# Kernel optimization log

Measured on AMD Instinct MI355X. Metric: run time of the kernel, lower is better.

The kernel has to match this reference:

```python
import jax, jax.numpy as jnp
import numpy as np

B = 16          # graphs per batch
NN = 2000       # nodes per graph (num_nodes)
N = B * NN      # total nodes in the batched graph
F_IN = 128      # input node features
H, C = 4, 64    # heads, per-head out channels (both GAT layers)
HC = H * C
DEG = 12        # average degree per node
FC1, FC2, OUT = 512, 128, 1
FC_IN = 6 * NN  # len(which_layer) = 6


def setup_inputs() -> dict:
    key = jax.random.key(0)
    ks = jax.random.split(key, 32)

    def g(i, shape, s=0.05):
        return jax.random.normal(ks[i], shape, jnp.float32) * s

    # within-graph random edges, no self loops (GATConv removes then re-adds them)
    src_l = jax.random.randint(ks[0], (B, NN * DEG), 0, NN)
    off = jax.random.randint(ks[1], (B, NN * DEG), 1, NN)
    dst_l = (src_l + off) % NN
    goff = (jnp.arange(B) * NN)[:, None]
    edge_index = jnp.stack([(src_l + goff).reshape(-1),
                            (dst_l + goff).reshape(-1)]).astype(jnp.int32)

    return {
        "x": g(2, (N, F_IN), 1.0),
        "W1": g(3, (F_IN, HC)), "att_src1": g(4, (H, C)), "att_dst1": g(5, (H, C)),
        "b1": jnp.zeros((HC,), jnp.float32),
        "W2": g(6, (HC, HC)), "att_src2": g(7, (H, C)), "att_dst2": g(8, (H, C)),
        "b2": jnp.zeros((HC,), jnp.float32),
        "pw1": g(9, (HC, 1)), "pb1": jnp.zeros((1,), jnp.float32),
        "pw2": g(10, (HC, 1)), "pb2": jnp.zeros((1,), jnp.float32),
        "ln_w": jnp.ones((NN,), jnp.float32), "ln_b": jnp.zeros((NN,), jnp.float32),
        "sex_emb": g(11, (2, NN)), "mut_emb": g(12, (4, NN)),
        "age_w": g(13, (NN,)), "age_b": jnp.zeros((NN,), jnp.float32),
        "fw1": g(14, (FC_IN, FC1)), "fb1": jnp.zeros((FC1,), jnp.float32),
        "fw2": g(15, (FC1, FC2)), "fb2": jnp.zeros((FC2,), jnp.float32),
        "fw3": g(16, (FC2, OUT)), "fb3": jnp.zeros((OUT,), jnp.float32),
        "age": jax.random.uniform(ks[17], (B,), jnp.float32),
        "edge_index": edge_index,
        "sex": jax.random.randint(ks[18], (B,), 0, 2),
        "mutation": jax.random.randint(ks[19], (B,), 0, 4),
    }


def _layer_norm(x, w, b, eps=1e-5):
    mu = jnp.mean(x, -1, keepdims=True)
    var = jnp.mean((x - mu) ** 2, -1, keepdims=True)
    return (x - mu) / jnp.sqrt(var + eps) * w + b


def _gat_conv(x, W, att_src, att_dst, bias, src, dst):
    h = (x @ W).reshape(N, H, C)                         # [N,H,C]
    a_s = jnp.sum(h * att_src[None], -1)                 # [N,H]
    a_d = jnp.sum(h * att_dst[None], -1)                 # [N,H]
    alpha = jax.nn.leaky_relu(a_s[src] + a_d[dst], 0.2)  # [E,H]
    m = jax.ops.segment_max(alpha, dst, num_segments=N)  # segment softmax over dst
    e = jnp.exp(alpha - m[dst])
    denom = jax.ops.segment_sum(e, dst, num_segments=N)
    a = e / (denom[dst] + 1e-16)
    out = jax.ops.segment_sum(a[:, :, None] * h[src], dst, num_segments=N)
    return out.reshape(N, HC) + bias


def _forward(x, W1, att_src1, att_dst1, b1, W2, att_src2, att_dst2, b2,
             pw1, pb1, pw2, pb2, ln_w, ln_b, sex_emb, mut_emb, age_w, age_b,
             fw1, fb1, fw2, fb2, fw3, fb3, age, edge_index, sex, mutation):
    loop = jnp.arange(N, dtype=edge_index.dtype)         # self loops added by GATConv
    src = jnp.concatenate([edge_index[0], loop])
    dst = jnp.concatenate([edge_index[1], loop])

    x0 = jnp.mean(x, -1).reshape(B, NN)                  # to_dense_batch(mean(x,-1))

    h = jax.nn.relu(_gat_conv(x, W1, att_src1, att_dst1, b1, src, dst))
    x1 = (h @ pw1 + pb1).squeeze(-1).reshape(B, NN)
    h = jax.nn.relu(_gat_conv(h, W2, att_src2, att_dst2, b2, src, dst))
    x2 = (h @ pw2 + pb2).squeeze(-1).reshape(B, NN)

    x0 = _layer_norm(x0, ln_w, ln_b)
    x1 = _layer_norm(x1, ln_w, ln_b)
    x2 = _layer_norm(x2, ln_w, ln_b)
    ms = jnp.concatenate([x0, x1, x2], axis=1)           # [B, 3*NN]

    demo = jnp.concatenate([sex_emb[sex], mut_emb[mutation],
                            age[:, None] * age_w[None, :] + age_b], axis=1)
    t = jnp.concatenate([demo, ms], axis=1)              # [B, 6*NN]
    t = jax.nn.relu(t @ fw1 + fb1)
    t = jax.nn.relu(t @ fw2 + fb2)
    pred = t @ fw3 + fb3                                 # [B, 1]
    return pred, x0, x1, x2, ms


def reference(x, W1, att_src1, att_dst1, b1, W2, att_src2, att_dst2, b2,
              pw1, pb1, pw2, pb2, ln_w, ln_b, sex_emb, mut_emb, age_w, age_b,
              fw1, fb1, fw2, fb2, fw3, fb3, age, edge_index, sex, mutation):
    return _forward(x, W1, att_src1, att_dst1, b1, W2, att_src2, att_dst2, b2,
                    pw1, pb1, pw2, pb2, ln_w, ln_b, sex_emb, mut_emb, age_w, age_b,
                    fw1, fb1, fw2, fb2, fw3, fb3, age, edge_index, sex, mutation)
```

## Files before the change

kernel.cpp:

```cpp
#include <hip/hip_runtime.h>
#include <math.h>

#define NTOT   32000
#define NNODE  2000
#define NB     16
#define FIN    128
#define HCDIM  256
#define NH     4
#define FC1DIM 512
#define FC2DIM 128
#define FCIN   12000
#define KC1    50
#define NCH1   240
#define CAP    64
#define BK     32
#define LPITCH 40
#define TRB    384
#define DEMOB  375

typedef __attribute__((ext_vector_type(8))) short bf16x8;
typedef __attribute__((ext_vector_type(4))) float f32x4;

__device__ inline float4 ld4(const float* p){ return *reinterpret_cast<const float4*>(p); }
__device__ inline void st4(float* p, float4 v){ *reinterpret_cast<float4*>(p) = v; }
__device__ inline float4 add4(float4 a, float4 b){ return make_float4(a.x+b.x,a.y+b.y,a.z+b.z,a.w+b.w); }
__device__ inline float lrelu(float x){ return x > 0.f ? x : 0.2f*x; }
__device__ inline float4 leaky4(float4 a){ return make_float4(lrelu(a.x),lrelu(a.y),lrelu(a.z),lrelu(a.w)); }
__device__ inline float4 exp4u(float4 a){ return make_float4(__expf(a.x),__expf(a.y),__expf(a.z),__expf(a.w)); }
__device__ inline float dot4(float4 a, float4 b){ return a.x*b.x + a.y*b.y + a.z*b.z + a.w*b.w; }
__device__ inline float selh(float4 v, int h){ return h==0 ? v.x : (h==1 ? v.y : (h==2 ? v.z : v.w)); }

__device__ inline unsigned short f2bf(float f){
  unsigned int u = __float_as_uint(f);
  u += 0x7FFFu + ((u >> 16) & 1u);
  return (unsigned short)(u >> 16);
}
__device__ inline unsigned int pk2bf(float a, float b){
  return (unsigned int)f2bf(a) | ((unsigned int)f2bf(b) << 16);
}
__device__ inline float bf2f(unsigned short h){
  return __uint_as_float(((unsigned int)h) << 16);
}
__device__ inline float4 ldbf4(const unsigned short* p){
  ushort4 v = *reinterpret_cast<const ushort4*>(p);
  return make_float4(bf2f(v.x), bf2f(v.y), bf2f(v.z), bf2f(v.w));
}

__global__ __launch_bounds__(256) void k_zero(int* __restrict__ cnt){
  int i = blockIdx.x*256 + threadIdx.x;
  if(i < NTOT) cnt[i] = 0;
}

__device__ __forceinline__ void ln_impl(const float* __restrict__ src,
                                        const float* __restrict__ lnw,
                                        const float* __restrict__ lnb,
                                        float* __restrict__ o1,
                                        float* __restrict__ o2,
                                        float* __restrict__ o3,
                                        float* red){
  int tid = threadIdx.x, lane = tid & 63, wv = tid >> 6;
  float s = 0.f, ss = 0.f;
  for(int i = tid; i < NNODE; i += 256){ float v = src[i]; s += v; ss += v*v; }
  #pragma unroll
  for(int off=1; off<64; off<<=1){ s += __shfl_xor(s, off); ss += __shfl_xor(ss, off); }
  if(lane == 0){ red[wv] = s; red[4+wv] = ss; }
  __syncthreads();
  s  = red[0]+red[1]+red[2]+red[3];
  ss = red[4]+red[5]+red[6]+red[7];
  float mu  = s * (1.0f/NNODE);
  float var = ss * (1.0f/NNODE) - mu*mu;
  float inv = 1.0f / sqrtf(var + 1e-5f);
  for(int i = tid; i < NNODE; i += 256){
    float v = (src[i]-mu)*inv*lnw[i] + lnb[i];
    o1[i] = v; o2[i] = v; o3[i] = v;
  }
}

__global__ void k_misc(const int* __restrict__ src, const int* __restrict__ dst,
                       int* __restrict__ cnt, int* __restrict__ col, int e0, int eb,
                       const float* __restrict__ W1, const float* __restrict__ W2,
                       unsigned short* __restrict__ W1t, unsigned short* __restrict__ W2t,
                       const float* __restrict__ sexemb, const float* __restrict__ mutemb,
                       const float* __restrict__ agew, const float* __restrict__ ageb,
                       const float* __restrict__ age, const int* __restrict__ sex,
                       const int* __restrict__ mut, float* __restrict__ t,
                       const float* __restrict__ x, float* __restrict__ x0r){
  int blk = blockIdx.x;
  if(blk < eb){
    int i = blk*256 + threadIdx.x;
    if(i < e0){
      int d = dst[i];
      int slot = atomicAdd(&cnt[d], 1);
      if(slot < CAP) col[(d<<6) + slot] = src[i];
    }
  } else if(blk < eb + TRB){
    int idx = (blk - eb)*256 + threadIdx.x;
    if(idx < HCDIM*FIN){
      int n = idx / FIN, k = idx - n*FIN;
      W1t[idx] = f2bf(W1[(size_t)k*HCDIM + n]);
    } else {
      int j = idx - HCDIM*FIN;
      int n = j / HCDIM, k = j - n*HCDIM;
      W2t[j] = f2bf(W2[(size_t)k*HCDIM + n]);
    }
  } else if(blk < eb + TRB + DEMOB){
    int i = (blk - eb - TRB)*256 + threadIdx.x;
    int b = i / (3*NNODE);
    int j = i - b*(3*NNODE);
    float v;
    if(j < NNODE)          v = sexemb[sex[b]*NNODE + j];
    else if(j < 2*NNODE)   v = mutemb[mut[b]*NNODE + (j - NNODE)];
    else                   v = age[b]*agew[j - 2*NNODE] + ageb[j - 2*NNODE];
    t[b*FCIN + j] = v;
  } else {
    int lane = threadIdx.x & 63, wv = threadIdx.x >> 6;
    int n = (blk - eb - TRB - DEMOB)*4 + wv;
    const float* r = x + (size_t)n*FIN;
    float2 v = *reinterpret_cast<const float2*>(r + lane*2);
    float s = v.x + v.y;
    #pragma unroll
    for(int off=1; off<64; off<<=1) s += __shfl_xor(s, off);
    if(lane == 0) x0r[n] = s * (1.0f/FIN);
  }
}

template<int AF32>
__global__ __launch_bounds__(256) void k_gemm_bf(const void* __restrict__ Av,
                                                 const unsigned short* __restrict__ Bt,
                                                 unsigned short* __restrict__ C,
                                                 const float* __restrict__ attS,
                                                 const float* __restrict__ attD,
                                                 float* __restrict__ a_s,
                                                 float* __restrict__ a_d,
                                                 int M, int K){
  const unsigned short* A = (const unsigned short*)Av;
  const float*         Af = (const float*)Av;
  __shared__ unsigned short As[128][LPITCH];
  __shared__ unsigned short Bs[128][LPITCH];
  int tid = threadIdx.x;
  int lane = tid & 63, wv = tid >> 6;
  int wm = (wv & 1)*64, wn = (wv >> 1)*64;
  int m0 = blockIdx.y*128, n0 = blockIdx.x*128;
  int l15 = lane & 15, lq = lane >> 4;
  f32x4 acc[4][4];
  #pragma unroll
  for(int i=0;i<4;i++)
    #pragma unroll
    for(int j=0;j<4;j++)
      acc[i][j] = (f32x4){0.f,0.f,0.f,0.f};

  int r = tid >> 2, c = (tid & 3)*8;
  for(int k0 = 0; k0 < K; k0 += BK){
    if(AF32){
      const float* pa  = Af + (size_t)(m0+r)*K + k0 + c;
      const float* pa2 = Af + (size_t)(m0+r+64)*K + k0 + c;
      float4 u0 = ld4(pa),  u1 = ld4(pa+4);
      float4 v0 = ld4(pa2), v1 = ld4(pa2+4);
      uint4 w0, w1;
      w0.x = pk2bf(u0.x,u0.y); w0.y = pk2bf(u0.z,u0.w);
      w0.z = pk2bf(u1.x,u1.y); w0.w = pk2bf(u1.z,u1.w);
      w1.x = pk2bf(v0.x,v0.y); w1.y = pk2bf(v0.z,v0.w);
      w1.z = pk2bf(v1.x,v1.y); w1.w = pk2bf(v1.z,v1.w);
      *reinterpret_cast<uint4*>(&As[r][c])    = w0;
      *reinterpret_cast<uint4*>(&As[r+64][c]) = w1;
    } else {
      *reinterpret_cast<uint4*>(&As[r][c])    = *reinterpret_cast<const uint4*>(A  + (size_t)(m0+r)*K + k0 + c);
      *reinterpret_cast<uint4*>(&As[r+64][c]) = *reinterpret_cast<const uint4*>(A  + (size_t)(m0+r+64)*K + k0 + c);
    }
    *reinterpret_cast<uint4*>(&Bs[r][c])    = *reinterpret_cast<const uint4*>(Bt + (size_t)(n0+r)*K + k0 + c);
    *reinterpret_cast<uint4*>(&Bs[r+64][c]) = *reinterpret_cast<const uint4*>(Bt + (size_t)(n0+r+64)*K + k0 + c);
    __syncthreads();
    bf16x8 af[4], bfr[4];
    #pragma unroll
    for(int i=0;i<4;i++){
      af[i]  = *reinterpret_cast<const bf16x8*>(&As[wm + i*16 + l15][lq*8]);
      bfr[i] = *reinterpret_cast<const bf16x8*>(&Bs[wn + i*16 + l15][lq*8]);
    }
    #pragma unroll
    for(int mi=0;mi<4;mi++)
      #pragma unroll
      for(int ni=0;ni<4;ni++)
        acc[mi][ni] = __builtin_amdgcn_mfma_f32_16x16x32_bf16(af[mi], bfr[ni], acc[mi][ni], 0, 0, 0);
    __syncthreads();
  }
  #pragma unroll
  for(int mi=0;mi<4;mi++){
    #pragma unroll
    for(int ni=0;ni<4;ni++){
      int cn = n0 + wn + ni*16 + l15;
      #pragma unroll
      for(int rg=0;rg<4;rg++){
        int rm = m0 + wm + mi*16 + lq*4 + rg;
        C[(size_t)rm*HCDIM + cn] = f2bf(acc[mi][ni][rg]);
      }
    }
  }
  int head = (n0 + wn) >> 6;
  float avs[4], avd[4];
  #pragma unroll
  for(int ni=0;ni<4;ni++){
    int cc = ni*16 + l15;
    avs[ni] = attS[head*64 + cc];
    avd[ni] = attD[head*64 + cc];
  }
  #pragma unroll
  for(int mi=0;mi<4;mi++){
    #pragma unroll
    for(int rg=0;rg<4;rg++){
      float ps = 0.f, pd = 0.f;
      #pragma unroll
      for(int ni=0;ni<4;ni++){
        float v = acc[mi][ni][rg];
        ps = fmaf(avs[ni], v, ps);
        pd = fmaf(avd[ni], v, pd);
      }
      #pragma unroll
      for(int off=1; off<16; off<<=1){
        ps += __shfl_xor(ps, off);
        pd += __shfl_xor(pd, off);
      }
      if(l15 == 0){
        int rm = m0 + wm + mi*16 + lq*4 + rg;
        a_s[rm*4 + head] = ps;
        a_d[rm*4 + head] = pd;
      }
    }
  }
}

template<int STORE>
__global__ __launch_bounds__(256) void k_agg(const unsigned short* __restrict__ hpre,
                                             const float* __restrict__ a_s,
                                             const float* __restrict__ a_d,
                                             const int* __restrict__ cnt,
                                             const int* __restrict__ col,
                                             const float* __restrict__ bias,
                                             const float* __restrict__ pw,
                                             const float* __restrict__ pb,
                                             unsigned short* __restrict__ hout,
                                             float* __restrict__ xraw,
                                             const float* __restrict__ lnsrc,
                                             const float* __restrict__ lnw,
                                             const float* __restrict__ lnb,
                                             float* __restrict__ out,
                                             float* __restrict__ t,
                                             int which){
  __shared__ float4 ew[4][CAP];
  __shared__ int    cols[4][CAP];
  __shared__ float  lred[8];
  int bx = blockIdx.x;
  if(bx < 16){
    int b = bx;
    ln_impl(lnsrc + b*NNODE, lnw, lnb,
            out + 16 + which*(NB*NNODE) + b*NNODE,
            out + 16 + 3*(NB*NNODE) + b*(3*NNODE) + which*NNODE,
            t + b*FCIN + 3*NNODE + which*NNODE, lred);
    return;
  }
  int tid = threadIdx.x;
  int lane = tid & 63, wv = tid >> 6;
  int blk  = bx - 16;
  int xcd  = blk & 7;
  int slot = blk >> 3;
  int half = slot / 500;
  int g    = xcd + 8*half;
  int n    = g*NNODE + (slot - half*500)*4 + wv;
  int f0 = lane*4;
  int hl = lane >> 4;
  float4 ad   = ld4(a_d + n*4);
  float4 asn  = ld4(a_s + n*4);
  float4 eself = exp4u(leaky4(add4(asn, ad)));
  int deg = min(cnt[n], CAP);
  int base = n << 6;
  if(lane < deg){
    int s = col[base + lane];
    cols[wv][lane] = s;
    ew[wv][lane] = exp4u(leaky4(add4(ld4(a_s + s*4), ad)));
  }
  float es = selh(eself, hl);
  float dsum = es;
  float4 hv = ldbf4(hpre + (size_t)n*HCDIM + f0);
  float4 acc = make_float4(es*hv.x, es*hv.y, es*hv.z, es*hv.w);
  const float* ewf = (const float*)&ew[wv][0];
  const int*   cwf = &cols[wv][0];
  for(int e = 0; e < deg; e++){
    int s = cwf[e];
    float w = ewf[e*4 + hl];
    dsum += w;
    float4 h2 = ldbf4(hpre + (size_t)s*HCDIM + f0);
    acc.x = fmaf(w, h2.x, acc.x); acc.y = fmaf(w, h2.y, acc.y);
    acc.z = fmaf(w, h2.z, acc.z); acc.w = fmaf(w, h2.w, acc.w);
  }
  float invh = 1.0f / (dsum + 1e-16f);
  float4 b4 = ld4(bias + f0);
  acc = make_float4(fmaxf(fmaf(acc.x,invh,b4.x),0.f), fmaxf(fmaf(acc.y,invh,b4.y),0.f),
                    fmaxf(fmaf(acc.z,invh,b4.z),0.f), fmaxf(fmaf(acc.w,invh,b4.w),0.f));
  if(STORE){
    ushort4 hb = make_ushort4(f2bf(acc.x), f2bf(acc.y), f2bf(acc.z), f2bf(acc.w));
    *reinterpret_cast<ushort4*>(hout + (size_t)n*HCDIM + f0) = hb;
  }
  float part = dot4(acc, ld4(pw + f0));
  #pragma unroll
  for(int off=1; off<64; off<<=1) part += __shfl_xor(part, off);
  if(lane == 0) xraw[n] = part + pb[0];
}

__global__ __launch_bounds__(256) void k_lnx2(const float* __restrict__ x2r,
                                              const float* __restrict__ lnw,
                                              const float* __restrict__ lnb,
                                              float* __restrict__ out,
                                              float* __restrict__ t){
  __shared__ float red[8];
  int b = blockIdx.x;
  ln_impl(x2r + b*NNODE, lnw, lnb,
          out + 16 + 2*(NB*NNODE) + b*NNODE,
          out + 16 + 3*(NB*NNODE) + b*(3*NNODE) + 2*NNODE,
          t + b*FCIN + 3*NNODE + 2*NNODE, red);
}

__global__ __launch_bounds__(256) void k_fc1p(const float* __restrict__ t,
                                              const float* __restrict__ fw1,
                                              float* __restrict__ partial){
  __shared__ float ts[NB][KC1];
  __shared__ float red[NB][FC1DIM];
  int tid = threadIdx.x;
  int half = tid >> 7;
  int c4 = (tid & 127) * 4;
  int k0 = blockIdx.x * KC1;
  for(int i = tid; i < NB*KC1; i += 256){
    int b = i / KC1, kk = i - b*KC1;
    ts[b][kk] = t[b*FCIN + k0 + kk];
  }
  __syncthreads();
  float4 acc[NB];
  #pragma unroll
  for(int b=0;b<NB;b++) acc[b] = make_float4(0.f,0.f,0.f,0.f);
  for(int kk = half; kk < KC1; kk += 2){
    float4 w = ld4(fw1 + (size_t)(k0+kk)*FC1DIM + c4);
    #pragma unroll
    for(int b=0;b<NB;b++){
      float tv = ts[b][kk];
      acc[b].x = fmaf(tv, w.x, acc[b].x);
      acc[b].y = fmaf(tv, w.y, acc[b].y);
      acc[b].z = fmaf(tv, w.z, acc[b].z);
      acc[b].w = fmaf(tv, w.w, acc[b].w);
    }
  }
  if(half == 1){
    #pragma unroll
    for(int b=0;b<NB;b++) st4(&red[b][c4], acc[b]);
  }
  __syncthreads();
  if(half == 0){
    float* po = partial + (size_t)blockIdx.x*(NB*FC1DIM);
    #pragma unroll
    for(int b=0;b<NB;b++){
      float4 r = ld4(&red[b][c4]);
      st4(po + b*FC1DIM + c4, add4(acc[b], r));
    }
  }
}

__global__ __launch_bounds__(256) void k_fc1r(const float* __restrict__ partial,
                                              const float* __restrict__ fb1,
                                              float* __restrict__ t1){
  __shared__ float red[3][64];
  int tid = threadIdx.x;
  int e = blockIdx.x*64 + (tid & 63);
  int g = tid >> 6;
  float s = 0.f;
  for(int c = g*60; c < g*60 + 60; c++) s += partial[(size_t)c*(NB*FC1DIM) + e];
  if(g) red[g-1][tid & 63] = s;
  __syncthreads();
  if(g == 0){
    s += red[0][tid & 63] + red[1][tid & 63] + red[2][tid & 63];
    s += fb1[e & (FC1DIM-1)];
    t1[e] = fmaxf(s, 0.f);
  }
}

__global__ __launch_bounds__(128) void k_head2(const float* __restrict__ t1,
                                               const float* __restrict__ fw2,
                                               const float* __restrict__ fb2,
                                               const float* __restrict__ fw3,
                                               const float* __restrict__ fb3,
                                               float* __restrict__ pred){
  __shared__ float red[2];
  int b = blockIdx.x, j = threadIdx.x;
  const float* tr = t1 + b*FC1DIM;
  float s = fb2[j];
  for(int k=0;k<FC1DIM;k++) s = fmaf(tr[k], fw2[k*FC2DIM+j], s);
  s = fmaxf(s, 0.f) * fw3[j];
  #pragma unroll
  for(int off=1; off<64; off<<=1) s += __shfl_xor(s, off);
  int lane = j & 63, wv = j >> 6;
  if(lane == 0) red[wv] = s;
  __syncthreads();
  if(j == 0) pred[b] = red[0] + red[1] + fb3[0];
}

extern "C" void kernel_launch(void* const* d_in, const int* in_sizes, int n_in,
                              void* d_out, int out_size, void* d_ws, size_t ws_size,
                              hipStream_t stream) {
  const float* x       = (const float*)d_in[0];
  const float* W1      = (const float*)d_in[1];
  const float* attS1   = (const float*)d_in[2];
  const float* attD1   = (const float*)d_in[3];
  const float* b1      = (const float*)d_in[4];
  const float* W2      = (const float*)d_in[5];
  const float* attS2   = (const float*)d_in[6];
  const float* attD2   = (const float*)d_in[7];
  const float* b2      = (const float*)d_in[8];
  const float* pw1     = (const float*)d_in[9];
  const float* pb1     = (const float*)d_in[10];
  const float* pw2     = (const float*)d_in[11];
  const float* pb2     = (const float*)d_in[12];
  const float* lnw     = (const float*)d_in[13];
  const float* lnb     = (const float*)d_in[14];
  const float* sexemb  = (const float*)d_in[15];
  const float* mutemb  = (const float*)d_in[16];
  const float* agew    = (const float*)d_in[17];
  const float* ageb    = (const float*)d_in[18];
  const float* fw1     = (const float*)d_in[19];
  const float* fb1     = (const float*)d_in[20];
  const float* fw2     = (const float*)d_in[21];
  const float* fb2     = (const float*)d_in[22];
  const float* fw3     = (const float*)d_in[23];
  const float* fb3     = (const float*)d_in[24];
  const float* age     = (const float*)d_in[25];
  const int*   eidx    = (const int*)d_in[26];
  const int*   sex     = (const int*)d_in[27];
  const int*   mut     = (const int*)d_in[28];
  const int E0 = in_sizes[26] / 2;
  const int* esrc = eidx;
  const int* edst = eidx + E0;

  float* out = (float*)d_out;

  float* w = (float*)d_ws;
  float* a_s  = w;
  float* a_d  = a_s + NTOT*NH;
  float* x0r  = a_d + NTOT*NH;
  float* x1r  = x0r + NTOT;
  float* x2r  = x1r + NTOT;
  float* tbuf = x2r + NTOT;
  float* part = tbuf + NB*FCIN;
  float* t1   = part + (size_t)NCH1*NB*FC1DIM;
  unsigned short* hA  = (unsigned short*)(t1 + NB*FC1DIM);
  unsigned short* hB  = hA  + (size_t)NTOT*HCDIM;
  unsigned short* W1t = hB  + (size_t)NTOT*HCDIM;
  unsigned short* W2t = W1t + HCDIM*FIN;
  int* cnt    = (int*)(W2t + HCDIM*HCDIM);
  int* col    = cnt + NTOT;
  (void)ws_size; (void)n_in; (void)out_size;

  const int eb = (E0 + 255)/256;

  k_zero<<<(NTOT+255)/256, 256, 0, stream>>>(cnt);
  k_misc<<<eb + TRB + DEMOB + NTOT/4, 256, 0, stream>>>(esrc, edst, cnt, col, E0, eb,
                                               W1, W2, W1t, W2t,
                                               sexemb, mutemb, agew, ageb,
                                               age, sex, mut, tbuf, x, x0r);

  k_gemm_bf<1><<<dim3(HCDIM/128, NTOT/128), 256, 0, stream>>>(x, W1t, hA, attS1, attD1, a_s, a_d, NTOT, FIN);
  k_agg<1><<<16 + NTOT/4, 256, 0, stream>>>(hA, a_s, a_d, cnt, col, b1, pw1, pb1, hB, x1r,
                                            x0r, lnw, lnb, out, tbuf, 0);

  k_gemm_bf<0><<<dim3(HCDIM/128, NTOT/128), 256, 0, stream>>>(hB, W2t, hA, attS2, attD2, a_s, a_d, NTOT, HCDIM);
  k_agg<0><<<16 + NTOT/4, 256, 0, stream>>>(hA, a_s, a_d, cnt, col, b2, pw2, pb2, hB, x2r,
                                            x1r, lnw, lnb, out, tbuf, 1);

  k_lnx2<<<NB, 256, 0, stream>>>(x2r, lnw, lnb, out, tbuf);

  k_fc1p<<<NCH1, 256, 0, stream>>>(tbuf, fw1, part);
  k_fc1r<<<(NB*FC1DIM)/64, 256, 0, stream>>>(part, fb1, t1);
  k_head2<<<NB, 128, 0, stream>>>(t1, fw2, fb2, fw3, fb3, out);
}
```

Before: 267.7 us.

## Widen GEMM tiles to full N, fold LayerNorm into FC1 and merge head kernels

The GEMM now uses 512-thread blocks that each cover all 256 output columns, so every A row tile is loaded and converted once instead of twice. The separate x2 LayerNorm kernel is removed: FC1 blocks that read the x2 range recompute per-graph mean and variance themselves and normalize on the fly, while 16 extra blocks write the LayerNorm outputs. The FC1 partial reduction and the FC2/FC3 head are merged into one kernel. This cuts three launches and one pass over the A input, at the cost of redundant statistics work in 40 FC1 blocks and a serial 240-chunk reduction inside only 16 head blocks.

```diff
diff --git a/kernel.cpp b/kernel.cpp
--- a/kernel.cpp
+++ b/kernel.cpp
@@ -72,7 +72,8 @@
   float inv = 1.0f / sqrtf(var + 1e-5f);
   for(int i = tid; i < NNODE; i += 256){
     float v = (src[i]-mu)*inv*lnw[i] + lnb[i];
-    o1[i] = v; o2[i] = v; o3[i] = v;
+    o1[i] = v; o2[i] = v;
+    if(o3) o3[i] = v;
   }
 }
 
@@ -125,7 +126,7 @@
 }
 
 template<int AF32>
-__global__ __launch_bounds__(256) void k_gemm_bf(const void* __restrict__ Av,
+__global__ __launch_bounds__(512) void k_gemm_bf(const void* __restrict__ Av,
                                                  const unsigned short* __restrict__ Bt,
                                                  unsigned short* __restrict__ C,
                                                  const float* __restrict__ attS,
@@ -136,11 +137,11 @@
   const unsigned short* A = (const unsigned short*)Av;
   const float*         Af = (const float*)Av;
   __shared__ unsigned short As[128][LPITCH];
-  __shared__ unsigned short Bs[128][LPITCH];
+  __shared__ unsigned short Bs[256][LPITCH];
   int tid = threadIdx.x;
   int lane = tid & 63, wv = tid >> 6;
-  int wm = (wv & 1)*64, wn = (wv >> 1)*64;
-  int m0 = blockIdx.y*128, n0 = blockIdx.x*128;
+  int wm = (wv >> 2)*64, wn = (wv & 3)*64;
+  int m0 = blockIdx.x*128;
   int l15 = lane & 15, lq = lane >> 4;
   f32x4 acc[4][4];
   #pragma unroll
@@ -149,26 +150,21 @@
     for(int j=0;j<4;j++)
       acc[i][j] = (f32x4){0.f,0.f,0.f,0.f};
 
-  int r = tid >> 2, c = (tid & 3)*8;
+  int r  = tid >> 2, c  = (tid & 3)*8;
+  int rb = tid >> 1, cb = (tid & 1)*16;
   for(int k0 = 0; k0 < K; k0 += BK){
     if(AF32){
-      const float* pa  = Af + (size_t)(m0+r)*K + k0 + c;
-      const float* pa2 = Af + (size_t)(m0+r+64)*K + k0 + c;
-      float4 u0 = ld4(pa),  u1 = ld4(pa+4);
-      float4 v0 = ld4(pa2), v1 = ld4(pa2+4);
-      uint4 w0, w1;
+      const float* pa = Af + (size_t)(m0+r)*K + k0 + c;
+      float4 u0 = ld4(pa), u1 = ld4(pa+4);
+      uint4 w0;
       w0.x = pk2bf(u0.x,u0.y); w0.y = pk2bf(u0.z,u0.w);
       w0.z = pk2bf(u1.x,u1.y); w0.w = pk2bf(u1.z,u1.w);
-      w1.x = pk2bf(v0.x,v0.y); w1.y = pk2bf(v0.z,v0.w);
-      w1.z = pk2bf(v1.x,v1.y); w1.w = pk2bf(v1.z,v1.w);
-      *reinterpret_cast<uint4*>(&As[r][c])    = w0;
-      *reinterpret_cast<uint4*>(&As[r+64][c]) = w1;
+      *reinterpret_cast<uint4*>(&As[r][c]) = w0;
     } else {
-      *reinterpret_cast<uint4*>(&As[r][c])    = *reinterpret_cast<const uint4*>(A  + (size_t)(m0+r)*K + k0 + c);
-      *reinterpret_cast<uint4*>(&As[r+64][c]) = *reinterpret_cast<const uint4*>(A  + (size_t)(m0+r+64)*K + k0 + c);
-    }
-    *reinterpret_cast<uint4*>(&Bs[r][c])    = *reinterpret_cast<const uint4*>(Bt + (size_t)(n0+r)*K + k0 + c);
-    *reinterpret_cast<uint4*>(&Bs[r+64][c]) = *reinterpret_cast<const uint4*>(Bt + (size_t)(n0+r+64)*K + k0 + c);
+      *reinterpret_cast<uint4*>(&As[r][c]) = *reinterpret_cast<const uint4*>(A + (size_t)(m0+r)*K + k0 + c);
+    }
+    *reinterpret_cast<uint4*>(&Bs[rb][cb])   = *reinterpret_cast<const uint4*>(Bt + (size_t)rb*K + k0 + cb);
+    *reinterpret_cast<uint4*>(&Bs[rb][cb+8]) = *reinterpret_cast<const uint4*>(Bt + (size_t)rb*K + k0 + cb + 8);
     __syncthreads();
     bf16x8 af[4], bfr[4];
     #pragma unroll
@@ -187,7 +183,7 @@
   for(int mi=0;mi<4;mi++){
     #pragma unroll
     for(int ni=0;ni<4;ni++){
-      int cn = n0 + wn + ni*16 + l15;
+      int cn = wn + ni*16 + l15;
       #pragma unroll
       for(int rg=0;rg<4;rg++){
         int rm = m0 + wm + mi*16 + lq*4 + rg;
@@ -195,7 +191,7 @@
       }
     }
   }
-  int head = (n0 + wn) >> 6;
+  int head = wn >> 6;
   float avs[4], avd[4];
   #pragma unroll
   for(int ni=0;ni<4;ni++){
@@ -305,33 +301,61 @@
   if(lane == 0) xraw[n] = part + pb[0];
 }
 
-__global__ __launch_bounds__(256) void k_lnx2(const float* __restrict__ x2r,
+__global__ __launch_bounds__(256) void k_fc1p(const float* __restrict__ t,
+                                              const float* __restrict__ x2r,
                                               const float* __restrict__ lnw,
                                               const float* __restrict__ lnb,
-                                              float* __restrict__ out,
-                                              float* __restrict__ t){
-  __shared__ float red[8];
-  int b = blockIdx.x;
-  ln_impl(x2r + b*NNODE, lnw, lnb,
-          out + 16 + 2*(NB*NNODE) + b*NNODE,
-          out + 16 + 3*(NB*NNODE) + b*(3*NNODE) + 2*NNODE,
-          t + b*FCIN + 3*NNODE + 2*NNODE, red);
-}
-
-__global__ __launch_bounds__(256) void k_fc1p(const float* __restrict__ t,
                                               const float* __restrict__ fw1,
-                                              float* __restrict__ partial){
+                                              float* __restrict__ partial,
+                                              float* __restrict__ out){
   __shared__ float ts[NB][KC1];
   __shared__ float red[NB][FC1DIM];
+  __shared__ float muv[NB], invv[NB];
+  __shared__ float lred[8];
+  int blk = blockIdx.x;
   int tid = threadIdx.x;
+
+  if(blk >= 240){
+    int b = blk - 240;
+    ln_impl(x2r + b*NNODE, lnw, lnb,
+            out + 16 + 2*(NB*NNODE) + b*NNODE,
+            out + 16 + 3*(NB*NNODE) + b*(3*NNODE) + 2*NNODE,
+            (float*)0, lred);
+    return;
+  }
+
+  int k0 = blk * KC1;
+  bool isx2 = (blk >= 200);
+  if(isx2){
+    int lane = tid & 63, wv = tid >> 6;
+    for(int q = 0; q < 4; q++){
+      int b = wv*4 + q;
+      const float* src = x2r + b*NNODE;
+      float s = 0.f, ss = 0.f;
+      for(int i = lane; i < NNODE; i += 64){ float v = src[i]; s += v; ss += v*v; }
+      #pragma unroll
+      for(int off=1; off<64; off<<=1){ s += __shfl_xor(s, off); ss += __shfl_xor(ss, off); }
+      if(lane == 0){
+        float mu  = s * (1.0f/NNODE);
+        float var = ss * (1.0f/NNODE) - mu*mu;
+        muv[b] = mu;
+        invv[b] = 1.0f / sqrtf(var + 1e-5f);
+      }
+    }
+    __syncthreads();
+  }
+  for(int i = tid; i < NB*KC1; i += 256){
+    int b = i / KC1, kk = i - b*KC1;
+    if(isx2){
+      int j = k0 + kk - 3*NNODE - 2*NNODE;
+      ts[b][kk] = (x2r[b*NNODE + j] - muv[b]) * invv[b] * lnw[j] + lnb[j];
+    } else {
+      ts[b][kk] = t[b*FCIN + k0 + kk];
+    }
+  }
+  __syncthreads();
   int half = tid >> 7;
   int c4 = (tid & 127) * 4;
-  int k0 = blockIdx.x * KC1;
-  for(int i = tid; i < NB*KC1; i += 256){
-    int b = i / KC1, kk = i - b*KC1;
-    ts[b][kk] = t[b*FCIN + k0 + kk];
-  }
-  __syncthreads();
   float4 acc[NB];
   #pragma unroll
   for(int b=0;b<NB;b++) acc[b] = make_float4(0.f,0.f,0.f,0.f);
@@ -352,7 +376,7 @@
   }
   __syncthreads();
   if(half == 0){
-    float* po = partial + (size_t)blockIdx.x*(NB*FC1DIM);
+    float* po = partial + (size_t)blk*(NB*FC1DIM);
     #pragma unroll
     for(int b=0;b<NB;b++){
       float4 r = ld4(&red[b][c4]);
@@ -361,42 +385,39 @@
   }
 }
 
-__global__ __launch_bounds__(256) void k_fc1r(const float* __restrict__ partial,
+__global__ __launch_bounds__(256) void k_head(const float* __restrict__ partial,
                                               const float* __restrict__ fb1,
-                                              float* __restrict__ t1){
-  __shared__ float red[3][64];
-  int tid = threadIdx.x;
-  int e = blockIdx.x*64 + (tid & 63);
-  int g = tid >> 6;
-  float s = 0.f;
-  for(int c = g*60; c < g*60 + 60; c++) s += partial[(size_t)c*(NB*FC1DIM) + e];
-  if(g) red[g-1][tid & 63] = s;
+                                              const float* __restrict__ fw2,
+                                              const float* __restrict__ fb2,
+                                              const float* __restrict__ fw3,
+                                              const float* __restrict__ fb3,
+                                              float* __restrict__ pred){
+  __shared__ float t1s[FC1DIM];
+  __shared__ float red[2];
+  int b = blockIdx.x, tid = threadIdx.x;
+  int e1 = tid, e2 = tid + 256;
+  float s1 = fb1[e1], s2 = fb1[e2];
+  const float* pb_ = partial + (size_t)b*FC1DIM;
+  for(int c = 0; c < NCH1; c++){
+    const float* pc = pb_ + (size_t)c*(NB*FC1DIM);
+    s1 += pc[e1];
+    s2 += pc[e2];
+  }
+  t1s[e1] = fmaxf(s1, 0.f);
+  t1s[e2] = fmaxf(s2, 0.f);
   __syncthreads();
-  if(g == 0){
-    s += red[0][tid & 63] + red[1][tid & 63] + red[2][tid & 63];
-    s += fb1[e & (FC1DIM-1)];
-    t1[e] = fmaxf(s, 0.f);
-  }
-}
-
-__global__ __launch_bounds__(128) void k_head2(const float* __restrict__ t1,
-                                               const float* __restrict__ fw2,
-                                               const float* __restrict__ fb2,
-                                               const float* __restrict__ fw3,
-                                               const float* __restrict__ fb3,
-                                               float* __restrict__ pred){
-  __shared__ float red[2];
-  int b = blockIdx.x, j = threadIdx.x;
-  const float* tr = t1 + b*FC1DIM;
-  float s = fb2[j];
-  for(int k=0;k<FC1DIM;k++) s = fmaf(tr[k], fw2[k*FC2DIM+j], s);
-  s = fmaxf(s, 0.f) * fw3[j];
-  #pragma unroll
-  for(int off=1; off<64; off<<=1) s += __shfl_xor(s, off);
-  int lane = j & 63, wv = j >> 6;
-  if(lane == 0) red[wv] = s;
+  if(tid < FC2DIM){
+    int j = tid;
+    float s = fb2[j];
+    for(int k = 0; k < FC1DIM; k++) s = fmaf(t1s[k], fw2[k*FC2DIM + j], s);
+    s = fmaxf(s, 0.f) * fw3[j];
+    #pragma unroll
+    for(int off=1; off<64; off<<=1) s += __shfl_xor(s, off);
+    int lane = j & 63, wv = j >> 6;
+    if(lane == 0) red[wv] = s;
+  }
   __syncthreads();
-  if(j == 0) pred[b] = red[0] + red[1] + fb3[0];
+  if(tid == 0) pred[b] = red[0] + red[1] + fb3[0];
 }
 
 extern "C" void kernel_launch(void* const* d_in, const int* in_sizes, int n_in,
@@ -462,17 +483,14 @@
                                                sexemb, mutemb, agew, ageb,
                                                age, sex, mut, tbuf, x, x0r);
 
-  k_gemm_bf<1><<<dim3(HCDIM/128, NTOT/128), 256, 0, stream>>>(x, W1t, hA, attS1, attD1, a_s, a_d, NTOT, FIN);
+  k_gemm_bf<1><<<NTOT/128, 512, 0, stream>>>(x, W1t, hA, attS1, attD1, a_s, a_d, NTOT, FIN);
   k_agg<1><<<16 + NTOT/4, 256, 0, stream>>>(hA, a_s, a_d, cnt, col, b1, pw1, pb1, hB, x1r,
                                             x0r, lnw, lnb, out, tbuf, 0);
 
-  k_gemm_bf<0><<<dim3(HCDIM/128, NTOT/128), 256, 0, stream>>>(hB, W2t, hA, attS2, attD2, a_s, a_d, NTOT, HCDIM);
+  k_gemm_bf<0><<<NTOT/128, 512, 0, stream>>>(hB, W2t, hA, attS2, attD2, a_s, a_d, NTOT, HCDIM);
   k_agg<0><<<16 + NTOT/4, 256, 0, stream>>>(hA, a_s, a_d, cnt, col, b2, pw2, pb2, hB, x2r,
                                             x1r, lnw, lnb, out, tbuf, 1);
 
-  k_lnx2<<<NB, 256, 0, stream>>>(x2r, lnw, lnb, out, tbuf);
-
-  k_fc1p<<<NCH1, 256, 0, stream>>>(tbuf, fw1, part);
-  k_fc1r<<<(NB*FC1DIM)/64, 256, 0, stream>>>(part, fb1, t1);
-  k_head2<<<NB, 128, 0, stream>>>(t1, fw2, fb2, fw3, fb3, out);
-}
+  k_fc1p<<<256, 256, 0, stream>>>(tbuf, x2r, lnw, lnb, fw1, part, out);
+  k_head<<<NB, 256, 0, stream>>>(part, fb1, fw2, fb2, fw3, fb3, out);
+}
```

After: 303.4 us. +13.4%, slower.

## Restructure FC1 split-K and fuse partial reduction into head kernel

Applied to the files above, without the earlier changes.

FC1 now uses 125 K-chunks of 96 rows, each split across two blocks by output half, with one scalar output column per thread instead of float4 columns and a shared-memory half-reduction. The separate partial-reduce kernel is folded into the FC2/FC3 head kernel, which sums the 125 partials per batch row itself, removing one launch and the t1 round trip. The trade-off is that the head now runs on only 16 blocks, each doing a serial 125-step reduction, and the FC1 weight loads are scalar rather than vectorized.

```diff
diff --git a/kernel.cpp b/kernel.cpp
--- a/kernel.cpp
+++ b/kernel.cpp
@@ -10,8 +10,8 @@
 #define FC1DIM 512
 #define FC2DIM 128
 #define FCIN   12000
-#define KC1    50
-#define NCH1   240
+#define NCH    125
+#define KCC    96
 #define CAP    64
 #define BK     32
 #define LPITCH 40
@@ -318,85 +318,70 @@
           t + b*FCIN + 3*NNODE + 2*NNODE, red);
 }
 
-__global__ __launch_bounds__(256) void k_fc1p(const float* __restrict__ t,
-                                              const float* __restrict__ fw1,
-                                              float* __restrict__ partial){
-  __shared__ float ts[NB][KC1];
-  __shared__ float red[NB][FC1DIM];
+__global__ __launch_bounds__(256) void k_fc1(const float* __restrict__ t,
+                                             const float* __restrict__ fw1,
+                                             float* __restrict__ partial){
+  __shared__ float ts[NB][KCC];
+  int blk = blockIdx.x;
+  int chunk = blk >> 1;
+  int halfc = blk & 1;
   int tid = threadIdx.x;
-  int half = tid >> 7;
-  int c4 = (tid & 127) * 4;
-  int k0 = blockIdx.x * KC1;
-  for(int i = tid; i < NB*KC1; i += 256){
-    int b = i / KC1, kk = i - b*KC1;
+  int k0 = chunk * KCC;
+  #pragma unroll
+  for(int i = tid; i < NB*KCC; i += 256){
+    int b = i / KCC, kk = i - b*KCC;
     ts[b][kk] = t[b*FCIN + k0 + kk];
   }
   __syncthreads();
-  float4 acc[NB];
-  #pragma unroll
-  for(int b=0;b<NB;b++) acc[b] = make_float4(0.f,0.f,0.f,0.f);
-  for(int kk = half; kk < KC1; kk += 2){
-    float4 w = ld4(fw1 + (size_t)(k0+kk)*FC1DIM + c4);
-    #pragma unroll
-    for(int b=0;b<NB;b++){
-      float tv = ts[b][kk];
-      acc[b].x = fmaf(tv, w.x, acc[b].x);
-      acc[b].y = fmaf(tv, w.y, acc[b].y);
-      acc[b].z = fmaf(tv, w.z, acc[b].z);
-      acc[b].w = fmaf(tv, w.w, acc[b].w);
-    }
-  }
-  if(half == 1){
-    #pragma unroll
-    for(int b=0;b<NB;b++) st4(&red[b][c4], acc[b]);
-  }
+  int j = halfc*256 + tid;
+  float acc[NB];
+  #pragma unroll
+  for(int b=0;b<NB;b++) acc[b] = 0.f;
+  const float* wp = fw1 + (size_t)k0*FC1DIM + j;
+  #pragma unroll 4
+  for(int kk = 0; kk < KCC; kk++){
+    float w = wp[(size_t)kk*FC1DIM];
+    #pragma unroll
+    for(int b=0;b<NB;b++) acc[b] = fmaf(ts[b][kk], w, acc[b]);
+  }
+  float* po = partial + (size_t)chunk*(NB*FC1DIM) + j;
+  #pragma unroll
+  for(int b=0;b<NB;b++) po[b*FC1DIM] = acc[b];
+}
+
+__global__ __launch_bounds__(256) void k_head(const float* __restrict__ partial,
+                                              const float* __restrict__ fb1,
+                                              const float* __restrict__ fw2,
+                                              const float* __restrict__ fb2,
+                                              const float* __restrict__ fw3,
+                                              const float* __restrict__ fb3,
+                                              float* __restrict__ pred){
+  __shared__ float t1s[FC1DIM];
+  __shared__ float red[2];
+  int b = blockIdx.x, tid = threadIdx.x;
+  int e1 = tid, e2 = tid + 256;
+  float s1 = fb1[e1], s2 = fb1[e2];
+  const float* pb_ = partial + (size_t)b*FC1DIM;
+  for(int c = 0; c < NCH; c++){
+    const float* pc = pb_ + (size_t)c*(NB*FC1DIM);
+    s1 += pc[e1];
+    s2 += pc[e2];
+  }
+  t1s[e1] = fmaxf(s1, 0.f);
+  t1s[e2] = fmaxf(s2, 0.f);
   __syncthreads();
-  if(half == 0){
-    float* po = partial + (size_t)blockIdx.x*(NB*FC1DIM);
-    #pragma unroll
-    for(int b=0;b<NB;b++){
-      float4 r = ld4(&red[b][c4]);
-      st4(po + b*FC1DIM + c4, add4(acc[b], r));
-    }
-  }
-}
-
-__global__ __launch_bounds__(256) void k_fc1r(const float* __restrict__ partial,
-                                              const float* __restrict__ fb1,
-                                              float* __restrict__ t1){
-  __shared__ float red[3][64];
-  int tid = threadIdx.x;
-  int e = blockIdx.x*64 + (tid & 63);
-  int g = tid >> 6;
-  float s = 0.f;
-  for(int c = g*60; c < g*60 + 60; c++) s += partial[(size_t)c*(NB*FC1DIM) + e];
-  if(g) red[g-1][tid & 63] = s;
+  if(tid < FC2DIM){
+    int j = tid;
+    float s = fb2[j];
+    for(int k = 0; k < FC1DIM; k++) s = fmaf(t1s[k], fw2[k*FC2DIM + j], s);
+    s = fmaxf(s, 0.f) * fw3[j];
+    #pragma unroll
+    for(int off=1; off<64; off<<=1) s += __shfl_xor(s, off);
+    int lane = j & 63, wv = j >> 6;
+    if(lane == 0) red[wv] = s;
+  }
   __syncthreads();
-  if(g == 0){
-    s += red[0][tid & 63] + red[1][tid & 63] + red[2][tid & 63];
-    s += fb1[e & (FC1DIM-1)];
-    t1[e] = fmaxf(s, 0.f);
-  }
-}
-
-__global__ __launch_bounds__(128) void k_head2(const float* __restrict__ t1,
-                                               const float* __restrict__ fw2,
-                                               const float* __restrict__ fb2,
-                                               const float* __restrict__ fw3,
-                                               const float* __restrict__ fb3,
-                                               float* __restrict__ pred){
-  __shared__ float red[2];
-  int b = blockIdx.x, j = threadIdx.x;
-  const float* tr = t1 + b*FC1DIM;
-  float s = fb2[j];
-  for(int k=0;k<FC1DIM;k++) s = fmaf(tr[k], fw2[k*FC2DIM+j], s);
-  s = fmaxf(s, 0.f) * fw3[j];
-  #pragma unroll
-  for(int off=1; off<64; off<<=1) s += __shfl_xor(s, off);
-  int lane = j & 63, wv = j >> 6;
-  if(lane == 0) red[wv] = s;
-  __syncthreads();
-  if(j == 0) pred[b] = red[0] + red[1] + fb3[0];
+  if(tid == 0) pred[b] = red[0] + red[1] + fb3[0];
 }
 
 extern "C" void kernel_launch(void* const* d_in, const int* in_sizes, int n_in,
@@ -445,7 +430,7 @@
   float* x2r  = x1r + NTOT;
   float* tbuf = x2r + NTOT;
   float* part = tbuf + NB*FCIN;
-  float* t1   = part + (size_t)NCH1*NB*FC1DIM;
+  float* t1   = part + (size_t)240*NB*FC1DIM;
   unsigned short* hA  = (unsigned short*)(t1 + NB*FC1DIM);
   unsigned short* hB  = hA  + (size_t)NTOT*HCDIM;
   unsigned short* W1t = hB  + (size_t)NTOT*HCDIM;
@@ -472,7 +457,6 @@
 
   k_lnx2<<<NB, 256, 0, stream>>>(x2r, lnw, lnb, out, tbuf);
 
-  k_fc1p<<<NCH1, 256, 0, stream>>>(tbuf, fw1, part);
-  k_fc1r<<<(NB*FC1DIM)/64, 256, 0, stream>>>(part, fb1, t1);
-  k_head2<<<NB, 128, 0, stream>>>(t1, fw2, fb2, fw3, fb3, out);
-}
+  k_fc1<<<NCH*2, 256, 0, stream>>>(tbuf, fw1, part);
+  k_head<<<NB, 256, 0, stream>>>(part, fb1, fw2, fb2, fw3, fb3, out);
+}
```

After: 276.3 us. 1.03x slower.
